# Kernel tuning notes

Hardware: AMD Instinct MI355X
Metric: run time of the kernel (lower is better)

The kernel has to match this reference:

```python
import jax, jax.numpy as jnp
import numpy as np

N = 16        # state dim n
M = 8         # control dim m
T = 50        # time_steps
DT = 0.01     # delta_t
SQRT_DT = DT ** 0.5
GAMMA = 0.1
SIGMA = 0.2
TAU = 0.5
H = 10        # hidden width of subnets
BATCH = 32768


def _mlp(params, x):
    W1, b1, W2, b2, W3, b3 = params
    h = jnp.tanh(x @ W1 + b1)
    h = jnp.tanh(h @ W2 + b2)
    return h @ W3 + b3


def setup_inputs() -> dict:
    key = jax.random.key(0)
    ks = jax.random.split(key, 32)

    def dense(k, i, o):
        return (jax.random.normal(k, (i, o), jnp.float32) / np.float32(np.sqrt(i)))

    inp = {
        'dw': jax.random.normal(ks[0], (T, BATCH, 1), jnp.float32) * SQRT_DT,
        'X0': jax.random.uniform(ks[1], (BATCH, N), jnp.float32),
        'A': dense(ks[2], N, N),
        'Bmat': dense(ks[3], N, M),
        'Cmat': dense(ks[4], N, N),
        'Dmat': dense(ks[5], N, M),
        # phi: (n+1) -> 10 -> 10 -> m
        'phi_W1': dense(ks[6], N + 1, H), 'phi_b1': jnp.zeros((H,), jnp.float32),
        'phi_W2': dense(ks[7], H, H),     'phi_b2': jnp.zeros((H,), jnp.float32),
        'phi_W3': dense(ks[8], H, M),     'phi_b3': jnp.zeros((M,), jnp.float32),
        # Z: (n+1) -> 10 -> 10 -> n
        'Z_W1': dense(ks[9], N + 1, H),   'Z_b1': jnp.zeros((H,), jnp.float32),
        'Z_W2': dense(ks[10], H, H),      'Z_b2': jnp.zeros((H,), jnp.float32),
        'Z_W3': dense(ks[11], H, N),      'Z_b3': jnp.zeros((N,), jnp.float32),
        # Y0: n -> 10 -> 10 -> n
        'Y0_W1': dense(ks[12], N, H),     'Y0_b1': jnp.zeros((H,), jnp.float32),
        'Y0_W2': dense(ks[13], H, H),     'Y0_b2': jnp.zeros((H,), jnp.float32),
        'Y0_W3': dense(ks[14], H, N),     'Y0_b3': jnp.zeros((N,), jnp.float32),
    }
    return inp


def reference(dw, X0, A, Bmat, Cmat, Dmat,
              phi_W1, phi_b1, phi_W2, phi_b2, phi_W3, phi_b3,
              Z_W1, Z_b1, Z_W2, Z_b2, Z_W3, Z_b3,
              Y0_W1, Y0_b1, Y0_W2, Y0_b2, Y0_W3, Y0_b3):
    phi_p = (phi_W1, phi_b1, phi_W2, phi_b2, phi_W3, phi_b3)
    Z_p = (Z_W1, Z_b1, Z_W2, Z_b2, Z_W3, Z_b3)
    Y0_p = (Y0_W1, Y0_b1, Y0_W2, Y0_b2, Y0_W3, Y0_b3)

    B = X0.shape[0]
    Y = _mlp(Y0_p, X0)                              # [B, n]
    t_grid = jnp.arange(T, dtype=X0.dtype) * DT     # [T]
    w_trap = jnp.ones((T,), X0.dtype).at[1:-1].set(2.0)  # trapezoid weights

    def step(carry, xs):
        X, Yc, lc = carry
        dwi, t, w = xs                              # dwi: [B,1]
        state = jnp.concatenate(
            [jnp.broadcast_to(t, (B, 1)).astype(X.dtype), X], axis=1)  # [B, n+1]
        Zv = _mlp(Z_p, state)                       # [B, n]
        u = _mlp(phi_p, state)                      # [B, m] (project = identity)
        # b_mult(M, x) == x @ M.T
        drift_X = X @ A.T + u @ Bmat.T + GAMMA      # [B, n]
        diffusion_X = X @ Cmat.T + u @ Dmat.T + SIGMA
        drift_Y = -(Yc @ A + Zv @ Cmat + X)         # f_x(X,u) = X
        # stop_recording branch: gradient of dH / pre_phi
        dH = Yc @ Bmat + Zv @ Dmat + u              # f_u(X,u) = u -> [B, m]
        pre_phi = jax.lax.stop_gradient(u - TAU * dH)
        Xn = X + drift_X * DT + dwi * diffusion_X
        Yn = Yc + drift_Y * DT + dwi * Zv
        lc = lc + 0.5 * DT * w * jnp.sum(jnp.square(u - pre_phi), axis=1)
        return (Xn, Yn, lc), None

    init = (X0, Y, jnp.zeros((B,), X0.dtype))
    (X, Y, loss_control), _ = jax.lax.scan(step, init, (dw, t_grid, w_trap))
    loss_bsde = jnp.sum(jnp.square(Y - X), axis=1)  # g_x(X) = X
    return jnp.stack([jnp.mean(loss_bsde), jnp.mean(loss_control)])
```

## Files before the change

### kernel.cpp

```cpp
#include <hip/hip_runtime.h>

namespace {

typedef float v4f __attribute__((ext_vector_type(4)));
typedef _Float16 half4 __attribute__((ext_vector_type(4)));
typedef unsigned int uint32;

constexpr int   kB     = 32768;
constexpr int   kT     = 50;
constexpr float kDT    = 0.01f;
constexpr float kGamma = 0.1f;
constexpr float kSigma = 0.2f;
constexpr float kTau   = 0.5f;
constexpr float kA     = 2.8853900817779268f;

constexpr int kNFrag      = 17;
constexpr int kFragDwords = kNFrag * 128;
constexpr int kBiasFloats = 11 * 16;

__device__ __forceinline__ float fact(float x) {
  return __builtin_amdgcn_rcpf(exp2f(x) + 1.0f);
}

__device__ __forceinline__ uint32 pk2(float a, float b) {
  union { _Float16 h[2]; uint32 u; } z;
  z.h[0] = (_Float16)a; z.h[1] = (_Float16)b;
  return z.u;
}

__device__ __forceinline__ v4f act4(v4f a) {
  v4f r;
  r[0] = fact(a[0]); r[1] = fact(a[1]);
  r[2] = fact(a[2]); r[3] = fact(a[3]);
  return r;
}

__global__ __launch_bounds__(256) void prep_kernel(
    const float* __restrict__ A,   const float* __restrict__ Bm,
    const float* __restrict__ Cm,  const float* __restrict__ Dm,
    const float* __restrict__ pW1, const float* __restrict__ pb1,
    const float* __restrict__ pW2, const float* __restrict__ pb2,
    const float* __restrict__ pW3, const float* __restrict__ pb3,
    const float* __restrict__ zW1, const float* __restrict__ zb1,
    const float* __restrict__ zW2, const float* __restrict__ zb2,
    const float* __restrict__ zW3, const float* __restrict__ zb3,
    const float* __restrict__ yW1, const float* __restrict__ yb1,
    const float* __restrict__ yW2, const float* __restrict__ yb2,
    const float* __restrict__ yW3, const float* __restrict__ yb3,
    uint32* __restrict__ ws, float* __restrict__ out)
{
  const int tid = threadIdx.x;
  if (tid < 2) out[tid] = 0.0f;

  auto sum10 = [](const float* W, int stride, int m) {
    float s = 0.f;
    for (int j = 0; j < 10; ++j) s += W[j * stride + m];
    return s;
  };

  auto wval = [&](int p, int m, int k) -> float {
    switch (p) {
      case 0:  return (m < 10) ? kA * yW1[k * 10 + m] : 0.f;
      case 1:  return (m < 10 && k < 10) ? -2.f * kA * yW2[k * 10 + m] : 0.f;
      case 2:  return (k < 10) ? -2.f * yW3[k * 16 + m] : 0.f;
      case 3:  return (m < 10) ? kA * zW1[(k + 1) * 10 + m] : 0.f;
      case 4:  return (m < 10) ? kA * pW1[(k + 1) * 10 + m] : 0.f;
      case 5:  return (m < 10 && k < 10) ? -2.f * kA * zW2[k * 10 + m] : 0.f;
      case 6:  return (m < 10 && k < 10) ? -2.f * kA * pW2[k * 10 + m] : 0.f;
      case 7:  return (k < 10) ? -2.f * zW3[k * 16 + m] : 0.f;
      case 8:  return (m < 8 && k < 10) ? -2.f * pW3[k * 8 + m] : 0.f;
      case 9:  return A[m * 16 + k];
      case 10: return (k < 8) ? Bm[m * 8 + k] : 0.f;
      case 11: return Cm[m * 16 + k];
      case 12: return (k < 8) ? Dm[m * 8 + k] : 0.f;
      case 13: return A[k * 16 + m];
      case 14: return Cm[k * 16 + m];
      case 15: return (m < 8) ? Bm[k * 8 + m] : 0.f;
      case 16: return (m < 8) ? Dm[k * 8 + m] : 0.f;
    }
    return 0.f;
  };

  for (int idx = tid; idx < kFragDwords; idx += 256) {
    int p = idx >> 7, r = idx & 127;
    int lane = r >> 1, dwi = r & 1;
    int m = lane & 15, q = lane >> 4;
    int k0 = 4 * q + 2 * dwi;
    ws[idx] = pk2(wval(p, m, k0), wval(p, m, k0 + 1));
  }

  float* bsf = (float*)(ws + kFragDwords);
  auto bval = [&](int a, int m) -> float {
    switch (a) {
      case 0:  return (m < 10) ? kA * yb1[m] : 0.f;
      case 1:  return (m < 10) ? kA * (yb2[m] + sum10(yW2, 10, m)) : 0.f;
      case 2:  return yb3[m] + sum10(yW3, 16, m);
      case 3:  return (m < 10) ? kA * (zb2[m] + sum10(zW2, 10, m)) : 0.f;
      case 4:  return (m < 10) ? kA * (pb2[m] + sum10(pW2, 10, m)) : 0.f;
      case 5:  return zb3[m] + sum10(zW3, 16, m);
      case 6:  return (m < 8) ? pb3[m] + sum10(pW3, 8, m) : 0.f;
      case 7:  return (m < 10) ? kA * zW1[m] : 0.f;
      case 8:  return (m < 10) ? kA * zb1[m] : 0.f;
      case 9:  return (m < 10) ? kA * pW1[m] : 0.f;
      case 10: return (m < 10) ? kA * pb1[m] : 0.f;
    }
    return 0.f;
  };
  for (int j = tid; j < kBiasFloats; j += 256) {
    bsf[j] = bval(j >> 4, j & 15);
  }
}

__global__ __launch_bounds__(64)
__attribute__((amdgpu_waves_per_eu(2, 2)))
void bsde_kernel(const float* __restrict__ dw, const float* __restrict__ X0,
                 const uint32* __restrict__ wsu, float* __restrict__ out)
{
  const int lane = threadIdx.x;
  const int col  = lane & 15;
  const int quad = lane >> 4;
  const int e    = blockIdx.x * 16 + col;
  const int bq   = quad * 4;

  half4 af[kNFrag];
#pragma unroll
  for (int p = 0; p < kNFrag; ++p) {
    union { uint2 u; half4 h; } z;
    z.u = *(const uint2*)(wsu + p * 128 + lane * 2);
    af[p] = z.h;
  }

  const float* bsf = (const float*)(wsu + kFragDwords);
  const v4f c2z = *(const v4f*)&bsf[3 * 16 + bq];
  const v4f c2p = *(const v4f*)&bsf[4 * 16 + bq];
  const v4f c3z = *(const v4f*)&bsf[5 * 16 + bq];
  const v4f c3p = *(const v4f*)&bsf[6 * 16 + bq];
  const v4f vtz = *(const v4f*)&bsf[7 * 16 + bq];
  const v4f vbz = *(const v4f*)&bsf[8 * 16 + bq];
  const v4f vtp = *(const v4f*)&bsf[9 * 16 + bq];
  const v4f vbp = *(const v4f*)&bsf[10 * 16 + bq];

  auto pk4 = [](v4f a) -> half4 {
    half4 h;
    h[0] = (_Float16)a[0]; h[1] = (_Float16)a[1];
    h[2] = (_Float16)a[2]; h[3] = (_Float16)a[3];
    return h;
  };
  auto mm = [](half4 a, half4 b, v4f c) -> v4f {
    return __builtin_amdgcn_mfma_f32_16x16x16f16(a, b, c, 0, 0, 0);
  };

  const v4f zero4 = {0.f, 0.f, 0.f, 0.f};
  const v4f gam4  = {kGamma, kGamma, kGamma, kGamma};
  const v4f sig4  = {kSigma, kSigma, kSigma, kSigma};

  v4f x4 = *(const v4f*)&X0[e * 16 + bq];
  half4 xB = pk4(x4);
  v4f y4;
  {
    v4f cy1 = *(const v4f*)&bsf[0 * 16 + bq];
    v4f cy2 = *(const v4f*)&bsf[1 * 16 + bq];
    v4f cy3 = *(const v4f*)&bsf[2 * 16 + bq];
    v4f h = mm(af[0], xB, cy1);
    v4f g = mm(af[1], pk4(act4(h)), cy2);
    y4    = mm(af[2], pk4(act4(g)), cy3);
  }

  float lcp = 0.0f;
  float dwv = dw[e];

#pragma unroll 1
  for (int t = 0; t < kT; ++t) {
    float dwn = (t < kT - 1) ? dw[(t + 1) * kB + e] : 0.0f;
    const float tv = (float)t * kDT;
    const float wt = (t == 0 || t == kT - 1) ? 1.0f : 2.0f;

    half4 yB = pk4(y4);

    v4f dx1 = mm(af[9],  xB, gam4);
    v4f fx1 = mm(af[11], xB, sig4);
    v4f dy1 = mm(af[13], yB, zero4);
    v4f dh1 = mm(af[15], yB, zero4);

    v4f c1z, c1p;
#pragma unroll
    for (int r = 0; r < 4; ++r) {
      c1z[r] = vbz[r] + tv * vtz[r];
      c1p[r] = vbp[r] + tv * vtp[r];
    }

    v4f hz = mm(af[3], xB, c1z);
    v4f hp = mm(af[4], xB, c1p);
    v4f gz = mm(af[5], pk4(act4(hz)), c2z);
    v4f gp = mm(af[6], pk4(act4(hp)), c2p);
    v4f zv = mm(af[7], pk4(act4(gz)), c3z);
    v4f uu = mm(af[8], pk4(act4(gp)), c3p);

    half4 zB = pk4(zv);
    half4 uB = pk4(uu);
    v4f dx = mm(af[10], uB, dx1);
    v4f fx = mm(af[12], uB, fx1);
    v4f dy = mm(af[14], zB, dy1);
    v4f dh = mm(af[16], zB, dh1);

    float ss = 0.0f;
    v4f Xn, Yn;
#pragma unroll
    for (int r = 0; r < 4; ++r) {
      Xn[r] = x4[r] + kDT * dx[r] + dwv * fx[r];
      Yn[r] = y4[r] - kDT * (dy[r] + x4[r]) + dwv * zv[r];
      float d = dh[r] + uu[r];
      ss += d * d;
    }
    lcp += (0.5f * kDT * kTau * kTau) * wt * ss;
    x4 = Xn; y4 = Yn;
    xB = pk4(x4);
    dwv = dwn;
  }

  float bp = 0.0f;
#pragma unroll
  for (int r = 0; r < 4; ++r) { float d = y4[r] - x4[r]; bp += d * d; }

#pragma unroll
  for (int s = 32; s > 0; s >>= 1) {
    bp  += __shfl_down(bp,  s, 64);
    lcp += __shfl_down(lcp, s, 64);
  }
  if (lane == 0) {
    atomicAdd(&out[0], bp  * (1.0f / (float)kB));
    atomicAdd(&out[1], lcp * (1.0f / (float)kB));
  }
}

}

extern "C" void kernel_launch(void* const* d_in, const int* in_sizes, int n_in,
                              void* d_out, int out_size, void* d_ws, size_t ws_size,
                              hipStream_t stream) {
  (void)in_sizes; (void)n_in; (void)ws_size; (void)out_size;

  const float* dw  = (const float*)d_in[0];
  const float* X0  = (const float*)d_in[1];
  const float* A   = (const float*)d_in[2];
  const float* Bm  = (const float*)d_in[3];
  const float* Cm  = (const float*)d_in[4];
  const float* Dm  = (const float*)d_in[5];
  const float* pW1 = (const float*)d_in[6];
  const float* pb1 = (const float*)d_in[7];
  const float* pW2 = (const float*)d_in[8];
  const float* pb2 = (const float*)d_in[9];
  const float* pW3 = (const float*)d_in[10];
  const float* pb3 = (const float*)d_in[11];
  const float* zW1 = (const float*)d_in[12];
  const float* zb1 = (const float*)d_in[13];
  const float* zW2 = (const float*)d_in[14];
  const float* zb2 = (const float*)d_in[15];
  const float* zW3 = (const float*)d_in[16];
  const float* zb3 = (const float*)d_in[17];
  const float* yW1 = (const float*)d_in[18];
  const float* yb1 = (const float*)d_in[19];
  const float* yW2 = (const float*)d_in[20];
  const float* yb2 = (const float*)d_in[21];
  const float* yW3 = (const float*)d_in[22];
  const float* yb3 = (const float*)d_in[23];
  float* out = (float*)d_out;
  unsigned int* ws = (unsigned int*)d_ws;

  prep_kernel<<<1, 256, 0, stream>>>(
      A, Bm, Cm, Dm,
      pW1, pb1, pW2, pb2, pW3, pb3,
      zW1, zb1, zW2, zb2, zW3, zb3,
      yW1, yb1, yW2, yb2, yW3, yb3, ws, out);

  bsde_kernel<<<kB / 16, 64, 0, stream>>>(dw, X0, ws, out);
}
```

Baseline: 191.2 us.

## Fold weight preprocessing into main kernel and use packed fp16 conversions

Removes the separate single-block prep kernel. Each wave now builds its fp16 MFMA weight fragments and folded biases directly from the raw weights, and the output is zeroed with a memset. It also swaps the exp2 and fp16 conversions for hardware builtins (cvt_pkrtz, amdgcn exp2) and folds the +X term of the Y drift into the MFMA accumulator. The cost is that every one of the 2048 blocks now does redundant scattered global loads and sum reductions in its prologue, and round-toward-zero conversion slightly changes numerics.

```diff
diff --git a/kernel.cpp b/kernel.cpp
--- a/kernel.cpp
+++ b/kernel.cpp
@@ -4,7 +4,7 @@
 
 typedef float v4f __attribute__((ext_vector_type(4)));
 typedef _Float16 half4 __attribute__((ext_vector_type(4)));
-typedef unsigned int uint32;
+typedef __fp16 fp16x2 __attribute__((ext_vector_type(2)));
 
 constexpr int   kB     = 32768;
 constexpr int   kT     = 50;
@@ -14,18 +14,17 @@
 constexpr float kTau   = 0.5f;
 constexpr float kA     = 2.8853900817779268f;
 
-constexpr int kNFrag      = 17;
-constexpr int kFragDwords = kNFrag * 128;
-constexpr int kBiasFloats = 11 * 16;
+
+__device__ __forceinline__ float fexp2(float x) {
+#if __has_builtin(__builtin_amdgcn_exp2f)
+  return __builtin_amdgcn_exp2f(x);
+#else
+  return exp2f(x);
+#endif
+}
 
 __device__ __forceinline__ float fact(float x) {
-  return __builtin_amdgcn_rcpf(exp2f(x) + 1.0f);
-}
-
-__device__ __forceinline__ uint32 pk2(float a, float b) {
-  union { _Float16 h[2]; uint32 u; } z;
-  z.h[0] = (_Float16)a; z.h[1] = (_Float16)b;
-  return z.u;
+  return __builtin_amdgcn_rcpf(fexp2(x) + 1.0f);
 }
 
 __device__ __forceinline__ v4f act4(v4f a) {
@@ -35,30 +34,30 @@
   return r;
 }
 
-__global__ __launch_bounds__(256) void prep_kernel(
-    const float* __restrict__ A,   const float* __restrict__ Bm,
-    const float* __restrict__ Cm,  const float* __restrict__ Dm,
-    const float* __restrict__ pW1, const float* __restrict__ pb1,
-    const float* __restrict__ pW2, const float* __restrict__ pb2,
-    const float* __restrict__ pW3, const float* __restrict__ pb3,
-    const float* __restrict__ zW1, const float* __restrict__ zb1,
-    const float* __restrict__ zW2, const float* __restrict__ zb2,
-    const float* __restrict__ zW3, const float* __restrict__ zb3,
-    const float* __restrict__ yW1, const float* __restrict__ yb1,
-    const float* __restrict__ yW2, const float* __restrict__ yb2,
-    const float* __restrict__ yW3, const float* __restrict__ yb3,
-    uint32* __restrict__ ws, float* __restrict__ out)
+__global__ __launch_bounds__(64)
+__attribute__((amdgpu_waves_per_eu(2, 2)))
+void bsde_kernel(const float* __restrict__ dw, const float* __restrict__ X0,
+                 const float* __restrict__ A,   const float* __restrict__ Bm,
+                 const float* __restrict__ Cm,  const float* __restrict__ Dm,
+                 const float* __restrict__ pW1, const float* __restrict__ pb1,
+                 const float* __restrict__ pW2, const float* __restrict__ pb2,
+                 const float* __restrict__ pW3, const float* __restrict__ pb3,
+                 const float* __restrict__ zW1, const float* __restrict__ zb1,
+                 const float* __restrict__ zW2, const float* __restrict__ zb2,
+                 const float* __restrict__ zW3, const float* __restrict__ zb3,
+                 const float* __restrict__ yW1, const float* __restrict__ yb1,
+                 const float* __restrict__ yW2, const float* __restrict__ yb2,
+                 const float* __restrict__ yW3, const float* __restrict__ yb3,
+                 float* __restrict__ out)
 {
-  const int tid = threadIdx.x;
-  if (tid < 2) out[tid] = 0.0f;
-
-  auto sum10 = [](const float* W, int stride, int m) {
-    float s = 0.f;
-    for (int j = 0; j < 10; ++j) s += W[j * stride + m];
-    return s;
-  };
-
-  auto wval = [&](int p, int m, int k) -> float {
+  const int lane = threadIdx.x;
+  const int col  = lane & 15;
+  const int quad = lane >> 4;
+  const int e    = blockIdx.x * 16 + col;
+  const int bq   = quad * 4;
+  const int m    = col;
+
+  auto wv = [&](int p, int k) -> float {
     switch (p) {
       case 0:  return (m < 10) ? kA * yW1[k * 10 + m] : 0.f;
       case 1:  return (m < 10 && k < 10) ? -2.f * kA * yW2[k * 10 + m] : 0.f;
@@ -81,89 +80,66 @@
     return 0.f;
   };
 
-  for (int idx = tid; idx < kFragDwords; idx += 256) {
-    int p = idx >> 7, r = idx & 127;
-    int lane = r >> 1, dwi = r & 1;
-    int m = lane & 15, q = lane >> 4;
-    int k0 = 4 * q + 2 * dwi;
-    ws[idx] = pk2(wval(p, m, k0), wval(p, m, k0 + 1));
-  }
-
-  float* bsf = (float*)(ws + kFragDwords);
-  auto bval = [&](int a, int m) -> float {
-    switch (a) {
-      case 0:  return (m < 10) ? kA * yb1[m] : 0.f;
-      case 1:  return (m < 10) ? kA * (yb2[m] + sum10(yW2, 10, m)) : 0.f;
-      case 2:  return yb3[m] + sum10(yW3, 16, m);
-      case 3:  return (m < 10) ? kA * (zb2[m] + sum10(zW2, 10, m)) : 0.f;
-      case 4:  return (m < 10) ? kA * (pb2[m] + sum10(pW2, 10, m)) : 0.f;
-      case 5:  return zb3[m] + sum10(zW3, 16, m);
-      case 6:  return (m < 8) ? pb3[m] + sum10(pW3, 8, m) : 0.f;
-      case 7:  return (m < 10) ? kA * zW1[m] : 0.f;
-      case 8:  return (m < 10) ? kA * zb1[m] : 0.f;
-      case 9:  return (m < 10) ? kA * pW1[m] : 0.f;
-      case 10: return (m < 10) ? kA * pb1[m] : 0.f;
-    }
-    return 0.f;
-  };
-  for (int j = tid; j < kBiasFloats; j += 256) {
-    bsf[j] = bval(j >> 4, j & 15);
-  }
-}
-
-__global__ __launch_bounds__(64)
-__attribute__((amdgpu_waves_per_eu(2, 2)))
-void bsde_kernel(const float* __restrict__ dw, const float* __restrict__ X0,
-                 const uint32* __restrict__ wsu, float* __restrict__ out)
-{
-  const int lane = threadIdx.x;
-  const int col  = lane & 15;
-  const int quad = lane >> 4;
-  const int e    = blockIdx.x * 16 + col;
-  const int bq   = quad * 4;
-
-  half4 af[kNFrag];
-#pragma unroll
-  for (int p = 0; p < kNFrag; ++p) {
-    union { uint2 u; half4 h; } z;
-    z.u = *(const uint2*)(wsu + p * 128 + lane * 2);
-    af[p] = z.h;
-  }
-
-  const float* bsf = (const float*)(wsu + kFragDwords);
-  const v4f c2z = *(const v4f*)&bsf[3 * 16 + bq];
-  const v4f c2p = *(const v4f*)&bsf[4 * 16 + bq];
-  const v4f c3z = *(const v4f*)&bsf[5 * 16 + bq];
-  const v4f c3p = *(const v4f*)&bsf[6 * 16 + bq];
-  const v4f vtz = *(const v4f*)&bsf[7 * 16 + bq];
-  const v4f vbz = *(const v4f*)&bsf[8 * 16 + bq];
-  const v4f vtp = *(const v4f*)&bsf[9 * 16 + bq];
-  const v4f vbp = *(const v4f*)&bsf[10 * 16 + bq];
+  half4 af[17];
+#pragma unroll
+  for (int p = 0; p < 17; ++p) {
+#pragma unroll
+    for (int j = 0; j < 4; ++j) af[p][j] = (_Float16)wv(p, 4 * quad + j);
+  }
+
+  auto sum10 = [](const float* W, int stride, int mm) {
+    float s = 0.f;
+#pragma unroll
+    for (int j = 0; j < 10; ++j) s += W[j * stride + mm];
+    return s;
+  };
+
+  v4f cy1, cy2, cy3, c2z, c2p, c3z, c3p, vtz, vbz, vtp, vbp;
+#pragma unroll
+  for (int r = 0; r < 4; ++r) {
+    const int mm = bq + r;
+    const bool m10 = mm < 10, m8 = mm < 8;
+    cy1[r] = m10 ? kA * yb1[mm] : 0.f;
+    cy2[r] = m10 ? kA * (yb2[mm] + sum10(yW2, 10, mm)) : 0.f;
+    cy3[r] = yb3[mm] + sum10(yW3, 16, mm);
+    c2z[r] = m10 ? kA * (zb2[mm] + sum10(zW2, 10, mm)) : 0.f;
+    c2p[r] = m10 ? kA * (pb2[mm] + sum10(pW2, 10, mm)) : 0.f;
+    c3z[r] = zb3[mm] + sum10(zW3, 16, mm);
+    c3p[r] = m8 ? (pb3[mm] + sum10(pW3, 8, mm)) : 0.f;
+    vtz[r] = m10 ? kA * zW1[mm] : 0.f;
+    vbz[r] = m10 ? kA * zb1[mm] : 0.f;
+    vtp[r] = m10 ? kA * pW1[mm] : 0.f;
+    vbp[r] = m10 ? kA * pb1[mm] : 0.f;
+  }
 
   auto pk4 = [](v4f a) -> half4 {
+#if __has_builtin(__builtin_amdgcn_cvt_pkrtz)
+    union { fp16x2 p[2]; half4 h; } z;
+    z.p[0] = __builtin_amdgcn_cvt_pkrtz(a[0], a[1]);
+    z.p[1] = __builtin_amdgcn_cvt_pkrtz(a[2], a[3]);
+    return z.h;
+#else
     half4 h;
     h[0] = (_Float16)a[0]; h[1] = (_Float16)a[1];
     h[2] = (_Float16)a[2]; h[3] = (_Float16)a[3];
     return h;
-  };
-  auto mm = [](half4 a, half4 b, v4f c) -> v4f {
+#endif
+  };
+  auto mm4 = [](half4 a, half4 b, v4f c) -> v4f {
     return __builtin_amdgcn_mfma_f32_16x16x16f16(a, b, c, 0, 0, 0);
   };
 
-  const v4f zero4 = {0.f, 0.f, 0.f, 0.f};
   const v4f gam4  = {kGamma, kGamma, kGamma, kGamma};
   const v4f sig4  = {kSigma, kSigma, kSigma, kSigma};
+  const v4f zero4 = {0.f, 0.f, 0.f, 0.f};
 
   v4f x4 = *(const v4f*)&X0[e * 16 + bq];
   half4 xB = pk4(x4);
   v4f y4;
   {
-    v4f cy1 = *(const v4f*)&bsf[0 * 16 + bq];
-    v4f cy2 = *(const v4f*)&bsf[1 * 16 + bq];
-    v4f cy3 = *(const v4f*)&bsf[2 * 16 + bq];
-    v4f h = mm(af[0], xB, cy1);
-    v4f g = mm(af[1], pk4(act4(h)), cy2);
-    y4    = mm(af[2], pk4(act4(g)), cy3);
+    v4f h = mm4(af[0], xB, cy1);
+    v4f g = mm4(af[1], pk4(act4(h)), cy2);
+    y4    = mm4(af[2], pk4(act4(g)), cy3);
   }
 
   float lcp = 0.0f;
@@ -177,10 +153,10 @@
 
     half4 yB = pk4(y4);
 
-    v4f dx1 = mm(af[9],  xB, gam4);
-    v4f fx1 = mm(af[11], xB, sig4);
-    v4f dy1 = mm(af[13], yB, zero4);
-    v4f dh1 = mm(af[15], yB, zero4);
+    v4f dx1 = mm4(af[9],  xB, gam4);
+    v4f fx1 = mm4(af[11], xB, sig4);
+    v4f dy1 = mm4(af[13], yB, x4);
+    v4f dh1 = mm4(af[15], yB, zero4);
 
     v4f c1z, c1p;
 #pragma unroll
@@ -189,26 +165,26 @@
       c1p[r] = vbp[r] + tv * vtp[r];
     }
 
-    v4f hz = mm(af[3], xB, c1z);
-    v4f hp = mm(af[4], xB, c1p);
-    v4f gz = mm(af[5], pk4(act4(hz)), c2z);
-    v4f gp = mm(af[6], pk4(act4(hp)), c2p);
-    v4f zv = mm(af[7], pk4(act4(gz)), c3z);
-    v4f uu = mm(af[8], pk4(act4(gp)), c3p);
+    v4f hz = mm4(af[3], xB, c1z);
+    v4f hp = mm4(af[4], xB, c1p);
+    v4f gz = mm4(af[5], pk4(act4(hz)), c2z);
+    v4f gp = mm4(af[6], pk4(act4(hp)), c2p);
+    v4f zv = mm4(af[7], pk4(act4(gz)), c3z);
+    v4f uu = mm4(af[8], pk4(act4(gp)), c3p);
 
     half4 zB = pk4(zv);
     half4 uB = pk4(uu);
-    v4f dx = mm(af[10], uB, dx1);
-    v4f fx = mm(af[12], uB, fx1);
-    v4f dy = mm(af[14], zB, dy1);
-    v4f dh = mm(af[16], zB, dh1);
+    v4f dx = mm4(af[10], uB, dx1);
+    v4f fx = mm4(af[12], uB, fx1);
+    v4f dy = mm4(af[14], zB, dy1);
+    v4f dh = mm4(af[16], zB, dh1);
 
     float ss = 0.0f;
     v4f Xn, Yn;
 #pragma unroll
     for (int r = 0; r < 4; ++r) {
       Xn[r] = x4[r] + kDT * dx[r] + dwv * fx[r];
-      Yn[r] = y4[r] - kDT * (dy[r] + x4[r]) + dwv * zv[r];
+      Yn[r] = y4[r] - kDT * dy[r] + dwv * zv[r];
       float d = dh[r] + uu[r];
       ss += d * d;
     }
@@ -238,7 +214,7 @@
 extern "C" void kernel_launch(void* const* d_in, const int* in_sizes, int n_in,
                               void* d_out, int out_size, void* d_ws, size_t ws_size,
                               hipStream_t stream) {
-  (void)in_sizes; (void)n_in; (void)ws_size; (void)out_size;
+  (void)in_sizes; (void)n_in; (void)ws_size; (void)out_size; (void)d_ws;
 
   const float* dw  = (const float*)d_in[0];
   const float* X0  = (const float*)d_in[1];
@@ -265,13 +241,12 @@
   const float* yW3 = (const float*)d_in[22];
   const float* yb3 = (const float*)d_in[23];
   float* out = (float*)d_out;
-  unsigned int* ws = (unsigned int*)d_ws;
-
-  prep_kernel<<<1, 256, 0, stream>>>(
-      A, Bm, Cm, Dm,
+
+  (void)hipMemsetAsync(out, 0, 2 * sizeof(float), stream);
+
+  bsde_kernel<<<kB / 16, 64, 0, stream>>>(
+      dw, X0, A, Bm, Cm, Dm,
       pW1, pb1, pW2, pb2, pW3, pb3,
       zW1, zb1, zW2, zb2, zW3, zb3,
-      yW1, yb1, yW2, yb2, yW3, yb3, ws, out);
-
-  bsde_kernel<<<kB / 16, 64, 0, stream>>>(dw, X0, ws, out);
-}
+      yW1, yb1, yW2, yb2, yW3, yb3, out);
+}
```

New measurement: 191.5 us. About the same (+0.2%).
